# Kernel tuning notes

Hardware: AMD Instinct MI355X
Metric: run time of the kernel (lower is better)

The kernel has to match this reference:

```python
import jax, jax.numpy as jnp
import numpy as np

N_HEAD = 16
D_MODEL = 2048

def setup_inputs() -> dict:
    key = jax.random.key(0)
    ks = jax.random.split(key, 9)
    B, T, C = 2, 2048, D_MODEL
    s = 1.0 / np.sqrt(C)
    return {
        "idx": jax.random.normal(ks[0], (B, T, C), dtype=jnp.float32),
        "Wq": jax.random.normal(ks[1], (C, C), dtype=jnp.float32) * s,
        "bq": jnp.zeros((C,), dtype=jnp.float32),
        "Wk": jax.random.normal(ks[2], (C, C), dtype=jnp.float32) * s,
        "bk": jnp.zeros((C,), dtype=jnp.float32),
        "Wv": jax.random.normal(ks[3], (C, C), dtype=jnp.float32) * s,
        "bv": jnp.zeros((C,), dtype=jnp.float32),
        "Wo": jax.random.normal(ks[4], (C, C), dtype=jnp.float32) * s,
        "bo": jnp.zeros((C,), dtype=jnp.float32),
    }

def reference(idx, Wq, bq, Wk, bk, Wv, bv, Wo, bo):
    B, T, C = idx.shape
    hs = C // N_HEAD
    def split_heads(x):
        return x.reshape(B, T, N_HEAD, hs).transpose(0, 2, 1, 3)  # [B,H,T,hs]
    q = split_heads(idx @ Wq + bq)
    k = split_heads(idx @ Wk + bk)
    v = split_heads(idx @ Wv + bv)
    scale = 1.0 / jnp.sqrt(jnp.asarray(hs, dtype=idx.dtype))
    scores = jnp.einsum('bhqd,bhkd->bhqk', q, k) * scale
    causal = jnp.tril(jnp.ones((T, T), dtype=bool))
    scores = jnp.where(causal, scores, -jnp.inf)
    attn = jax.nn.softmax(scores, axis=-1)
    out = jnp.einsum('bhqk,bhkd->bhqd', attn, v)
    out = out.transpose(0, 2, 1, 3).reshape(B, T, C)
    return out @ Wo + bo
```

## Files before the change

### kernel.cpp

```cpp
#include <hip/hip_runtime.h>
#include <hip/hip_bf16.h>

#define TT 2048
#define CC 2048
#define HH 16
#define HS 128
#define BB 2
#define MM (BB*TT)

typedef __attribute__((ext_vector_type(8))) short bf16x8;
typedef __attribute__((ext_vector_type(4))) short bf16x4;
typedef __attribute__((ext_vector_type(4))) float f32x4;
typedef __attribute__((ext_vector_type(16))) float f32x16;

__device__ __forceinline__ short f2bf(float x) {
    unsigned u = __float_as_uint(x);
    unsigned r = (u + 0x7FFFu + ((u >> 16) & 1u)) >> 16;
    return (short)r;
}

__device__ __forceinline__ void gl_lds16(const void* g, void* l) {
    __builtin_amdgcn_global_load_lds(
        (const __attribute__((address_space(1))) unsigned int*)g,
        (__attribute__((address_space(3))) unsigned int*)l,
        16, 0, 0);
}

__global__ void cvt_bf16_kernel(const float* __restrict__ x, short* __restrict__ y, int n) {
    int stride = gridDim.x * blockDim.x;
    for (int i = blockIdx.x * blockDim.x + threadIdx.x; i < n/4; i += stride) {
        float4 v = reinterpret_cast<const float4*>(x)[i];
        bf16x4 s;
        s[0] = f2bf(v.x); s[1] = f2bf(v.y); s[2] = f2bf(v.z); s[3] = f2bf(v.w);
        reinterpret_cast<bf16x4*>(y)[i] = s;
    }
}

__global__ void wt_kernel(const float* __restrict__ w0, const float* __restrict__ w1,
                          const float* __restrict__ w2, const float* __restrict__ w3,
                          short* __restrict__ o0, short* __restrict__ o1,
                          short* __restrict__ o2, short* __restrict__ o3)
{
    const float* W; short* Wt;
    switch (blockIdx.z) {
        case 0:  W = w0; Wt = o0; break;
        case 1:  W = w1; Wt = o1; break;
        case 2:  W = w2; Wt = o2; break;
        default: W = w3; Wt = o3; break;
    }
    __shared__ float tile[32][33];
    int tx = threadIdx.x, ty = threadIdx.y;
    int k0 = blockIdx.x * 32, n0 = blockIdx.y * 32;
    #pragma unroll
    for (int i = 0; i < 4; ++i)
        tile[ty + i*8][tx] = W[(size_t)(k0 + ty + i*8) * CC + n0 + tx];
    __syncthreads();
    #pragma unroll
    for (int i = 0; i < 4; ++i)
        Wt[(size_t)(n0 + ty + i*8) * CC + k0 + tx] = f2bf(tile[tx][ty + i*8]);
}

__launch_bounds__(512)
__global__ void gemm_qkv3_kernel(const short* __restrict__ A, const short* __restrict__ Wcat,
                                 const float* __restrict__ bq, const float* __restrict__ bk,
                                 const float* __restrict__ bv,
                                 short* __restrict__ Qd, short* __restrict__ Kd,
                                 short* __restrict__ Vtd, float qscale)
{
    __shared__ __align__(16) short As[256*64];
    __shared__ __align__(16) short Bs[128*64];
    const int tid = threadIdx.x;
    const int lane = tid & 63;
    const int g = lane >> 4, fr = lane & 15;
    const int wid = tid >> 6;
    const int wm = wid >> 1, wn = wid & 1;

    const int bid = blockIdx.x;
    const int m0  = (bid & 15) * 256;
    const int nt0 = bid >> 4;
    const short* Bt = Wcat + (size_t)nt0 * 128 * CC;

    f32x4 acc[4][4];
    #pragma unroll
    for (int i = 0; i < 4; ++i)
        #pragma unroll
        for (int j = 0; j < 4; ++j) acc[i][j] = (f32x4){0.f,0.f,0.f,0.f};

    for (int k0 = 0; k0 < CC; k0 += 64) {
        __syncthreads();
        #pragma unroll
        for (int i = 0; i < 4; ++i) {
            int c = i*512 + tid;
            int row = c >> 3;
            int kbl = ((c & 7) * 16) ^ ((row & 7) << 4);
            gl_lds16(reinterpret_cast<const char*>(A) + ((size_t)(m0+row)*CC + k0)*2 + kbl,
                     reinterpret_cast<char*>(As) + c*16);
        }
        #pragma unroll
        for (int i = 0; i < 2; ++i) {
            int c = i*512 + tid;
            int row = c >> 3;
            int kbl = ((c & 7) * 16) ^ ((row & 7) << 4);
            gl_lds16(reinterpret_cast<const char*>(Bt) + ((size_t)row*CC + k0)*2 + kbl,
                     reinterpret_cast<char*>(Bs) + c*16);
        }
        __syncthreads();
        #pragma unroll
        for (int cch = 0; cch < 2; ++cch) {
            bf16x8 a[4], b[4];
            #pragma unroll
            for (int i = 0; i < 4; ++i) {
                int row = wm*64 + i*16 + fr;
                int kph = (cch*64 + g*16) ^ ((row & 7) << 4);
                a[i] = *reinterpret_cast<const bf16x8*>(
                    reinterpret_cast<const char*>(As) + row*128 + kph);
            }
            #pragma unroll
            for (int j = 0; j < 4; ++j) {
                int row = wn*64 + j*16 + fr;
                int kph = (cch*64 + g*16) ^ ((row & 7) << 4);
                b[j] = *reinterpret_cast<const bf16x8*>(
                    reinterpret_cast<const char*>(Bs) + row*128 + kph);
            }
            #pragma unroll
            for (int i = 0; i < 4; ++i)
                #pragma unroll
                for (int j = 0; j < 4; ++j)
                    acc[i][j] = __builtin_amdgcn_mfma_f32_16x16x32_bf16(a[i], b[j], acc[i][j], 0, 0, 0);
        }
    }

    const int sec = nt0 >> 4;
    const float scl = (sec == 0) ? qscale : 1.0f;
    const float* bp = (sec == 0) ? bq : ((sec == 1) ? bk : bv);
    #pragma unroll
    for (int j = 0; j < 4; ++j) {
        int nn = (nt0 & 15)*128 + wn*64 + j*16 + fr;
        float bval = bp[nn];
        int h = nn >> 7, d = nn & (HS-1);
        #pragma unroll
        for (int i = 0; i < 4; ++i) {
            #pragma unroll
            for (int r = 0; r < 4; ++r) {
                int mg = m0 + wm*64 + i*16 + g*4 + r;
                int bb = mg >> 11, tq = mg & (TT-1);
                short ov = f2bf((acc[i][j][r] + bval) * scl);
                if (sec == 0)      Qd [((size_t)(bb*HH + h)*TT + tq)*HS + d] = ov;
                else if (sec == 1) Kd [((size_t)(bb*HH + h)*TT + tq)*HS + d] = ov;
                else               Vtd[((size_t)(bb*HH + h)*HS + d)*TT + tq] = ov;
            }
        }
    }
}

__launch_bounds__(256)
__global__ void gemm_out_kernel(const short* __restrict__ A, const short* __restrict__ Bt,
                                const float* __restrict__ bias, float* __restrict__ dst)
{
    __shared__ __align__(16) short As[128*64];
    __shared__ __align__(16) short Bs[128*64];
    const int tid = threadIdx.x;
    const int lane = tid & 63;
    const int g = lane >> 4, fr = lane & 15;
    const int wid = tid >> 6;
    const int wr = wid >> 1, wc = wid & 1;

    const int bid = blockIdx.x;
    const int m0 = (bid & 31) * 128;
    const int n0 = (bid >> 5) * 128;

    f32x4 acc[4][4];
    #pragma unroll
    for (int i = 0; i < 4; ++i)
        #pragma unroll
        for (int j = 0; j < 4; ++j) acc[i][j] = (f32x4){0.f,0.f,0.f,0.f};

    for (int k0 = 0; k0 < CC; k0 += 64) {
        __syncthreads();
        #pragma unroll
        for (int i = 0; i < 4; ++i) {
            int c = i*256 + tid;
            int row = c >> 3;
            int kbl = ((c & 7) * 16) ^ ((row & 7) << 4);
            gl_lds16(reinterpret_cast<const char*>(A) + ((size_t)(m0+row)*CC + k0)*2 + kbl,
                     reinterpret_cast<char*>(As) + c*16);
        }
        #pragma unroll
        for (int i = 0; i < 4; ++i) {
            int c = i*256 + tid;
            int row = c >> 3;
            int kbl = ((c & 7) * 16) ^ ((row & 7) << 4);
            gl_lds16(reinterpret_cast<const char*>(Bt) + ((size_t)(n0+row)*CC + k0)*2 + kbl,
                     reinterpret_cast<char*>(Bs) + c*16);
        }
        __syncthreads();
        #pragma unroll
        for (int cch = 0; cch < 2; ++cch) {
            bf16x8 a[4], b[4];
            #pragma unroll
            for (int i = 0; i < 4; ++i) {
                int row = wr*64 + i*16 + fr;
                int kph = (cch*64 + g*16) ^ ((row & 7) << 4);
                a[i] = *reinterpret_cast<const bf16x8*>(
                    reinterpret_cast<const char*>(As) + row*128 + kph);
            }
            #pragma unroll
            for (int j = 0; j < 4; ++j) {
                int row = wc*64 + j*16 + fr;
                int kph = (cch*64 + g*16) ^ ((row & 7) << 4);
                b[j] = *reinterpret_cast<const bf16x8*>(
                    reinterpret_cast<const char*>(Bs) + row*128 + kph);
            }
            #pragma unroll
            for (int i = 0; i < 4; ++i)
                #pragma unroll
                for (int j = 0; j < 4; ++j)
                    acc[i][j] = __builtin_amdgcn_mfma_f32_16x16x32_bf16(a[i], b[j], acc[i][j], 0, 0, 0);
        }
    }

    #pragma unroll
    for (int j = 0; j < 4; ++j) {
        int n = n0 + wc*64 + j*16 + fr;
        float bval = bias[n];
        #pragma unroll
        for (int i = 0; i < 4; ++i)
            #pragma unroll
            for (int r = 0; r < 4; ++r) {
                int m = m0 + wr*64 + i*16 + g*4 + r;
                dst[(size_t)m*CC + n] = acc[i][j][r] + bval;
            }
    }
}

__launch_bounds__(256, 2)
__global__ void attn_kernel(const short* __restrict__ Q, const short* __restrict__ K,
                            const short* __restrict__ Vt, short* __restrict__ O)
{
    __shared__ __align__(16) short Ks[2][64*128];
    __shared__ __align__(16) short Vs[2][128*64];

    const int tid = threadIdx.x;
    const int lane = tid & 63;
    const int wid = tid >> 6;
    const int l5 = lane >> 5;
    const int q31 = lane & 31;
    const bool hif = (l5 != 0);

    const int dd = blockIdx.x;
    const int g8 = dd & 7;
    const int s  = (dd >> 3) & 31;
    const int half = dd >> 8;
    const int bh = g8*4 + (s >> 3);
    const int u  = s & 7;
    const int qb = half ? u : (15 - u);
    const int q0 = qb * 128;
    const int wq0 = q0 + wid*32;

    const short* Qh = Q + (size_t)bh * TT * HS;
    const char*  Kg = (const char*)(K  + (size_t)bh * TT * HS);
    const char*  Vg = (const char*)(Vt + (size_t)bh * HS * TT);

    bf16x8 qf[8];
    #pragma unroll
    for (int dk = 0; dk < 8; ++dk)
        qf[dk] = *reinterpret_cast<const bf16x8*>(
            Qh + (size_t)(wq0 + q31)*HS + dk*16 + l5*8);

    f32x16 o[4];
    #pragma unroll
    for (int c = 0; c < 4; ++c)
        #pragma unroll
        for (int r = 0; r < 16; ++r) o[c][r] = 0.f;
    float mrun = -1e30f, lrun = 0.f;

    auto stage = [&](int kv0, int p) {
        char* Kd = reinterpret_cast<char*>(Ks[p]);
        char* Vd = reinterpret_cast<char*>(Vs[p]);
        #pragma unroll
        for (int i = 0; i < 4; ++i) {
            int c = i*256 + tid;
            int row = c >> 4;
            int lg  = ((c & 15) * 16) ^ ((row & 7) << 4);
            gl_lds16(Kg + (size_t)(kv0 + row)*256 + lg, Kd + c*16);
        }
        #pragma unroll
        for (int i = 0; i < 4; ++i) {
            int c = i*256 + tid;
            int row = c >> 3;
            int lg  = ((c & 7) * 16) ^ ((row & 7) << 4);
            gl_lds16(Vg + ((size_t)row*TT + kv0)*2 + lg, Vd + c*16);
        }
    };

    const int nst = q0/64 + 2;
    stage(0, 0);

    for (int t = 0; t < nst; ++t) {
        const int kv0 = t * 64;
        __syncthreads();
        if (t + 1 < nst) stage(kv0 + 64, (t+1) & 1);

        if (kv0 > wq0 + 31) continue;

        const char* Kl = reinterpret_cast<const char*>(Ks[t & 1]);
        const char* Vl = reinterpret_cast<const char*>(Vs[t & 1]);

        f32x16 st[2];
        #pragma unroll
        for (int t2 = 0; t2 < 2; ++t2)
            #pragma unroll
            for (int r = 0; r < 16; ++r) st[t2][r] = 0.f;
        __builtin_amdgcn_s_setprio(1);
        #pragma unroll
        for (int t2 = 0; t2 < 2; ++t2) {
            int krow = t2*32 + q31;
            int rsw = (krow & 7) << 4;
            #pragma unroll
            for (int dk = 0; dk < 8; ++dk) {
                bf16x8 kf = *reinterpret_cast<const bf16x8*>(
                    Kl + krow*256 + ((dk*32 + l5*16) ^ rsw));
                st[t2] = __builtin_amdgcn_mfma_f32_32x32x16_bf16(kf, qf[dk], st[t2], 0, 0, 0);
            }
        }
        __builtin_amdgcn_s_setprio(0);
        if (kv0 + 63 > wq0) {
            int qrow = wq0 + q31;
            #pragma unroll
            for (int t2 = 0; t2 < 2; ++t2)
                #pragma unroll
                for (int r = 0; r < 16; ++r) {
                    int kv = kv0 + t2*32 + (r & 3) + ((r >> 2) << 3) + l5*4;
                    if (kv > qrow) st[t2][r] = -1e30f;
                }
        }
        float pm = -1e30f;
        #pragma unroll
        for (int t2 = 0; t2 < 2; ++t2)
            #pragma unroll
            for (int r = 0; r < 16; ++r) pm = fmaxf(pm, st[t2][r]);
        if (__any(pm > mrun + 8.f)) {
            float pmf = fmaxf(pm, __shfl_xor(pm, 32));
            float mn = fmaxf(mrun, pmf);
            float al = __builtin_amdgcn_exp2f(mrun - mn);
            mrun = mn; lrun *= al;
            #pragma unroll
            for (int c = 0; c < 4; ++c)
                #pragma unroll
                for (int r = 0; r < 16; ++r) o[c][r] *= al;
        }
        float ps = 0.f;
        #pragma unroll
        for (int t2 = 0; t2 < 2; ++t2)
            #pragma unroll
            for (int r = 0; r < 16; ++r) {
                float pv = __builtin_amdgcn_exp2f(st[t2][r] - mrun);
                st[t2][r] = pv;
                ps += pv;
            }
        lrun += ps;
        unsigned pw[2][8];
        #pragma unroll
        for (int t2 = 0; t2 < 2; ++t2)
            #pragma unroll
            for (int w = 0; w < 8; ++w)
                asm("v_cvt_pk_bf16_f32 %0, %1, %2"
                    : "=v"(pw[t2][w]) : "v"(st[t2][2*w]), "v"(st[t2][2*w+1]));
        #pragma unroll
        for (int c4 = 0; c4 < 4; ++c4) {
            int t2 = c4 >> 1, b0 = (c4 & 1) * 4;
            unsigned A0 = pw[t2][b0+0], A1 = pw[t2][b0+1];
            unsigned A2 = pw[t2][b0+2], A3 = pw[t2][b0+3];
            unsigned X0 = (unsigned)__shfl_xor((int)A0, 32);
            unsigned X1 = (unsigned)__shfl_xor((int)A1, 32);
            unsigned X2 = (unsigned)__shfl_xor((int)A2, 32);
            unsigned X3 = (unsigned)__shfl_xor((int)A3, 32);
            union { unsigned u[4]; bf16x8 v; } fu;
            fu.u[0] = hif ? X2 : A0;
            fu.u[1] = hif ? X3 : A1;
            fu.u[2] = hif ? A2 : X0;
            fu.u[3] = hif ? A3 : X1;
            __builtin_amdgcn_s_setprio(1);
            #pragma unroll
            for (int c = 0; c < 4; ++c) {
                int vrow = c*32 + q31;
                bf16x8 vf = *reinterpret_cast<const bf16x8*>(
                    Vl + vrow*128 + ((c4*32 + l5*16) ^ ((vrow & 7) << 4)));
                o[c] = __builtin_amdgcn_mfma_f32_32x32x16_bf16(vf, fu.v, o[c], 0, 0, 0);
            }
            __builtin_amdgcn_s_setprio(0);
        }
    }

    lrun += __shfl_xor(lrun, 32);
    float inv = 1.f / lrun;
    int b = bh >> 4, h = bh & 15;
    size_t base = ((size_t)(b*TT + wq0 + q31))*CC + (size_t)h*HS;
    #pragma unroll
    for (int c = 0; c < 4; ++c)
        #pragma unroll
        for (int g2 = 0; g2 < 4; ++g2) {
            bf16x4 v4;
            #pragma unroll
            for (int j = 0; j < 4; ++j) v4[j] = f2bf(o[c][g2*4 + j] * inv);
            *reinterpret_cast<bf16x4*>(O + base + c*32 + g2*8 + l5*4) = v4;
        }
}

extern "C" void kernel_launch(void* const* d_in, const int* in_sizes, int n_in,
                              void* d_out, int out_size, void* d_ws, size_t ws_size,
                              hipStream_t stream)
{
    const float* idx = (const float*)d_in[0];
    const float* Wq  = (const float*)d_in[1];
    const float* bq  = (const float*)d_in[2];
    const float* Wk  = (const float*)d_in[3];
    const float* bk  = (const float*)d_in[4];
    const float* Wv  = (const float*)d_in[5];
    const float* bv  = (const float*)d_in[6];
    const float* Wo  = (const float*)d_in[7];
    const float* bo  = (const float*)d_in[8];
    float* out = (float*)d_out;

    short* Xbf  = (short*)d_ws;
    short* Wcat = Xbf  + (size_t)MM*CC;
    short* Wto  = Wcat + (size_t)3*CC*CC;
    short* Qb   = Wto  + (size_t)CC*CC;
    short* Kb   = Qb   + (size_t)MM*CC;
    short* Vtb  = Kb   + (size_t)MM*CC;
    short* Ob   = Vtb  + (size_t)MM*CC;

    cvt_bf16_kernel<<<1024, 256, 0, stream>>>(idx, Xbf, MM*CC);
    wt_kernel<<<dim3(CC/32, CC/32, 4), dim3(32, 8), 0, stream>>>(
        Wq, Wk, Wv, Wo,
        Wcat, Wcat + (size_t)CC*CC, Wcat + (size_t)2*CC*CC, Wto);

    const float qs = 0.08838834764831845f * 1.4426950408889634f;
    gemm_qkv3_kernel<<<dim3(768), 512, 0, stream>>>(Xbf, Wcat, bq, bk, bv, Qb, Kb, Vtb, qs);

    attn_kernel<<<dim3(512), 256, 0, stream>>>(Qb, Kb, Vtb, Ob);

    gemm_out_kernel<<<dim3(512), 256, 0, stream>>>(Ob, Wto, bo, out);
}
```

Measured before the change: 271.8 us.

## Rewrite QKV GEMM as 256x256 tile with double-buffered 8-phase pipelined LDS loads

Replaces the QKV projection GEMM with a 256x256 output tile per block, using double-buffered LDS staging split into half-tiles. Global-to-LDS loads for later K steps are interleaved with MFMA phases, paced by fine-grained vmcnt waits, raw barriers and setprio. The larger tile halves the grid and raises operand reuse per loaded byte. In exchange it uses 128KB of LDS and many registers, allowing one block per CU, and relies on the hand-written wait counts being correct.

```diff
diff --git a/kernel.cpp b/kernel.cpp
--- a/kernel.cpp
+++ b/kernel.cpp
@@ -25,6 +25,14 @@
         (__attribute__((address_space(3))) unsigned int*)l,
         16, 0, 0);
 }
+
+__device__ __forceinline__ void rbar() {
+    asm volatile("" ::: "memory");
+    __builtin_amdgcn_s_barrier();
+    asm volatile("" ::: "memory");
+}
+#define VM4  asm volatile("s_waitcnt vmcnt(4)" ::: "memory")
+#define VM0  asm volatile("s_waitcnt vmcnt(0)" ::: "memory")
 
 __global__ void cvt_bf16_kernel(const float* __restrict__ x, short* __restrict__ y, int n) {
     int stride = gridDim.x * blockDim.x;
@@ -60,97 +68,149 @@
         Wt[(size_t)(n0 + ty + i*8) * CC + k0 + tx] = f2bf(tile[tx][ty + i*8]);
 }
 
-__launch_bounds__(512)
-__global__ void gemm_qkv3_kernel(const short* __restrict__ A, const short* __restrict__ Wcat,
+__launch_bounds__(512, 1)
+__global__ void gemm_qkv8_kernel(const short* __restrict__ A, const short* __restrict__ Wcat,
                                  const float* __restrict__ bq, const float* __restrict__ bk,
                                  const float* __restrict__ bv,
                                  short* __restrict__ Qd, short* __restrict__ Kd,
                                  short* __restrict__ Vtd, float qscale)
 {
-    __shared__ __align__(16) short As[256*64];
-    __shared__ __align__(16) short Bs[128*64];
+    __shared__ __align__(16) short As[2][256*64];
+    __shared__ __align__(16) short Bs[2][256*64];
+
     const int tid = threadIdx.x;
     const int lane = tid & 63;
     const int g = lane >> 4, fr = lane & 15;
     const int wid = tid >> 6;
-    const int wm = wid >> 1, wn = wid & 1;
+    const int wm = wid >> 2, wn = wid & 3;
 
     const int bid = blockIdx.x;
-    const int m0  = (bid & 15) * 256;
-    const int nt0 = bid >> 4;
-    const short* Bt = Wcat + (size_t)nt0 * 128 * CC;
-
-    f32x4 acc[4][4];
-    #pragma unroll
-    for (int i = 0; i < 4; ++i)
-        #pragma unroll
-        for (int j = 0; j < 4; ++j) acc[i][j] = (f32x4){0.f,0.f,0.f,0.f};
-
-    for (int k0 = 0; k0 < CC; k0 += 64) {
-        __syncthreads();
-        #pragma unroll
-        for (int i = 0; i < 4; ++i) {
-            int c = i*512 + tid;
-            int row = c >> 3;
-            int kbl = ((c & 7) * 16) ^ ((row & 7) << 4);
-            gl_lds16(reinterpret_cast<const char*>(A) + ((size_t)(m0+row)*CC + k0)*2 + kbl,
-                     reinterpret_cast<char*>(As) + c*16);
-        }
+    const int m0 = (bid & 15) * 256;
+    const int n0 = (bid >> 4) * 256;
+
+    const char* Ab = (const char*)A;
+    const char* Bb = (const char*)(Wcat + (size_t)n0 * CC);
+
+    auto stageA = [&](int h, int tt, int b) {
+        if (tt >= CC/64) return;
+        char* dst = (char*)As[b];
         #pragma unroll
         for (int i = 0; i < 2; ++i) {
-            int c = i*512 + tid;
-            int row = c >> 3;
-            int kbl = ((c & 7) * 16) ^ ((row & 7) << 4);
-            gl_lds16(reinterpret_cast<const char*>(Bt) + ((size_t)row*CC + k0)*2 + kbl,
-                     reinterpret_cast<char*>(Bs) + c*16);
-        }
-        __syncthreads();
-        #pragma unroll
-        for (int cch = 0; cch < 2; ++cch) {
-            bf16x8 a[4], b[4];
-            #pragma unroll
-            for (int i = 0; i < 4; ++i) {
-                int row = wm*64 + i*16 + fr;
-                int kph = (cch*64 + g*16) ^ ((row & 7) << 4);
-                a[i] = *reinterpret_cast<const bf16x8*>(
-                    reinterpret_cast<const char*>(As) + row*128 + kph);
-            }
-            #pragma unroll
-            for (int j = 0; j < 4; ++j) {
-                int row = wn*64 + j*16 + fr;
-                int kph = (cch*64 + g*16) ^ ((row & 7) << 4);
-                b[j] = *reinterpret_cast<const bf16x8*>(
-                    reinterpret_cast<const char*>(Bs) + row*128 + kph);
-            }
-            #pragma unroll
-            for (int i = 0; i < 4; ++i)
+            int c  = i*512 + tid;
+            int rh = c >> 3;
+            int row = (rh & 63) + h*64 + (rh >> 6)*128;
+            int kb  = (c & 7) * 16;
+            gl_lds16(Ab + ((size_t)(m0 + row)*CC + tt*64)*2 + (kb ^ ((row & 7) << 4)),
+                     dst + row*128 + kb);
+        }
+    };
+    auto stageB = [&](int nc, int tt, int b) {
+        if (tt >= CC/64) return;
+        char* dst = (char*)Bs[b];
+        #pragma unroll
+        for (int i = 0; i < 2; ++i) {
+            int c  = i*512 + tid;
+            int rb = c >> 3;
+            int row = (rb & 31) + nc*32 + (rb >> 5)*64;
+            int kb  = (c & 7) * 16;
+            gl_lds16(Bb + ((size_t)row*CC + tt*64)*2 + (kb ^ ((row & 7) << 4)),
+                     dst + row*128 + kb);
+        }
+    };
+
+    f32x4 acc[2][2][4][2];
+    #pragma unroll
+    for (int mr = 0; mr < 2; ++mr)
+        #pragma unroll
+        for (int nc = 0; nc < 2; ++nc)
+            #pragma unroll
+            for (int m = 0; m < 4; ++m)
                 #pragma unroll
-                for (int j = 0; j < 4; ++j)
-                    acc[i][j] = __builtin_amdgcn_mfma_f32_16x16x32_bf16(a[i], b[j], acc[i][j], 0, 0, 0);
-        }
+                for (int n = 0; n < 2; ++n)
+                    acc[mr][nc][m][n] = (f32x4){0.f,0.f,0.f,0.f};
+
+    bf16x8 a[4][2], b0[2][2], b1[2][2];
+    const char* A0l = (const char*)As[0];
+    const char* A1l = (const char*)As[1];
+    const char* B0l = (const char*)Bs[0];
+    const char* B1l = (const char*)Bs[1];
+
+#define QLDA(AL, MR) { \
+    _Pragma("unroll") for (int m_ = 0; m_ < 4; ++m_) { \
+        _Pragma("unroll") for (int kk_ = 0; kk_ < 2; ++kk_) { \
+            int row_ = wm*128 + (MR)*64 + m_*16 + fr; \
+            a[m_][kk_] = *(const bf16x8*)((AL) + row_*128 + ((kk_*64 + g*16) ^ ((row_ & 7) << 4))); \
+        } } }
+#define QLDB(BL, NC, BB_) { \
+    _Pragma("unroll") for (int n_ = 0; n_ < 2; ++n_) { \
+        _Pragma("unroll") for (int kk_ = 0; kk_ < 2; ++kk_) { \
+            int row_ = wn*64 + (NC)*32 + n_*16 + fr; \
+            BB_[n_][kk_] = *(const bf16x8*)((BL) + row_*128 + ((kk_*64 + g*16) ^ ((row_ & 7) << 4))); \
+        } } }
+#define QMM(MR, NC, BB_) { \
+    __builtin_amdgcn_s_setprio(1); \
+    _Pragma("unroll") for (int m_ = 0; m_ < 4; ++m_) { \
+        _Pragma("unroll") for (int n_ = 0; n_ < 2; ++n_) { \
+            _Pragma("unroll") for (int kk_ = 0; kk_ < 2; ++kk_) { \
+                acc[MR][NC][m_][n_] = __builtin_amdgcn_mfma_f32_16x16x32_bf16( \
+                    a[m_][kk_], BB_[n_][kk_], acc[MR][NC][m_][n_], 0, 0, 0); \
+        } } } \
+    __builtin_amdgcn_s_setprio(0); }
+
+    stageA(0, 0, 0); stageB(0, 0, 0); stageB(1, 0, 0); stageA(1, 0, 0);
+    stageA(0, 1, 1); stageB(0, 1, 1); stageB(1, 1, 1);
+    VM0;
+    rbar();
+
+    const int NI = CC/128;
+    #pragma unroll 1
+    for (int i = 0; i < NI; ++i) {
+        const int t1 = 2*i + 1, t2 = 2*i + 2, t3 = 2*i + 3;
+        VM4; QLDA(A0l, 0); QLDB(B0l, 0, b0); stageA(1, t1, 1);
+        rbar(); QMM(0, 0, b0); rbar();
+        VM4; QLDB(B0l, 1, b1); stageA(0, t2, 0);
+        rbar(); QMM(0, 1, b1); rbar();
+        VM4; QLDA(A0l, 1); stageB(0, t2, 0);
+        rbar(); QMM(1, 0, b0); rbar();
+        VM4; stageB(1, t2, 0);
+        rbar(); QMM(1, 1, b1); rbar();
+        VM4; QLDA(A1l, 0); QLDB(B1l, 0, b0); stageA(1, t2, 0);
+        rbar(); QMM(0, 0, b0); rbar();
+        VM4; QLDB(B1l, 1, b1); stageA(0, t3, 1);
+        rbar(); QMM(0, 1, b1); rbar();
+        VM4; QLDA(A1l, 1); stageB(0, t3, 1);
+        rbar(); QMM(1, 0, b0); rbar();
+        VM4; stageB(1, t3, 1);
+        rbar(); QMM(1, 1, b1); rbar();
     }
-
-    const int sec = nt0 >> 4;
+#undef QLDA
+#undef QLDB
+#undef QMM
+
+    const int sec = n0 >> 11;
     const float scl = (sec == 0) ? qscale : 1.0f;
     const float* bp = (sec == 0) ? bq : ((sec == 1) ? bk : bv);
     #pragma unroll
-    for (int j = 0; j < 4; ++j) {
-        int nn = (nt0 & 15)*128 + wn*64 + j*16 + fr;
-        float bval = bp[nn];
-        int h = nn >> 7, d = nn & (HS-1);
-        #pragma unroll
-        for (int i = 0; i < 4; ++i) {
-            #pragma unroll
-            for (int r = 0; r < 4; ++r) {
-                int mg = m0 + wm*64 + i*16 + g*4 + r;
-                int bb = mg >> 11, tq = mg & (TT-1);
-                short ov = f2bf((acc[i][j][r] + bval) * scl);
-                if (sec == 0)      Qd [((size_t)(bb*HH + h)*TT + tq)*HS + d] = ov;
-                else if (sec == 1) Kd [((size_t)(bb*HH + h)*TT + tq)*HS + d] = ov;
-                else               Vtd[((size_t)(bb*HH + h)*HS + d)*TT + tq] = ov;
-            }
-        }
-    }
+    for (int mr = 0; mr < 2; ++mr)
+        #pragma unroll
+        for (int nc = 0; nc < 2; ++nc)
+            #pragma unroll
+            for (int n = 0; n < 2; ++n) {
+                int nn = (n0 & 2047) + wn*64 + nc*32 + n*16 + fr;
+                float bval = bp[nn];
+                int h = nn >> 7, d = nn & (HS-1);
+                #pragma unroll
+                for (int m = 0; m < 4; ++m)
+                    #pragma unroll
+                    for (int r = 0; r < 4; ++r) {
+                        int mg = m0 + wm*128 + mr*64 + m*16 + g*4 + r;
+                        int bb2 = mg >> 11, tq = mg & (TT-1);
+                        short ov = f2bf((acc[mr][nc][m][n][r] + bval) * scl);
+                        if (sec == 0)      Qd [((size_t)(bb2*HH + h)*TT + tq)*HS + d] = ov;
+                        else if (sec == 1) Kd [((size_t)(bb2*HH + h)*TT + tq)*HS + d] = ov;
+                        else               Vtd[((size_t)(bb2*HH + h)*HS + d)*TT + tq] = ov;
+                    }
+            }
 }
 
 __launch_bounds__(256)
@@ -436,7 +496,7 @@
         Wcat, Wcat + (size_t)CC*CC, Wcat + (size_t)2*CC*CC, Wto);
 
     const float qs = 0.08838834764831845f * 1.4426950408889634f;
-    gemm_qkv3_kernel<<<dim3(768), 512, 0, stream>>>(Xbf, Wcat, bq, bk, bv, Qb, Kb, Vtb, qs);
+    gemm_qkv8_kernel<<<dim3(384), 512, 0, stream>>>(Xbf, Wcat, bq, bk, bv, Qb, Kb, Vtb, qs);
 
     attn_kernel<<<dim3(512), 256, 0, stream>>>(Qb, Kb, Vtb, Ob);
 
```

Result: slower. 286.6 us (+5.4%).
